# Kernel optimization log

Measured on AMD Instinct MI355X. Metric: run time of the kernel, lower is better.

Reference implementation:

```python
import jax, jax.numpy as jnp
import numpy as np

B = 1
E = 8388608                      # embedding size (dim 1)
NNZ = 131072                     # inhibition links
MIN_SPARSITY = 0.002
MAX_SPARSITY = 0.02
BOOST_PERCENT = 1e-8             # forward default boost_percent
MAX_ACTIVE = int(np.ceil(MAX_SPARSITY * E))    # 167773, torch uses .item() -> static
MIN_ACTIVE = int(np.floor(MIN_SPARSITY * E))   # 16777


def setup_inputs() -> dict:
    key = jax.random.key(0)
    k1, k3, k4, k5 = jax.random.split(key, 4)
    x = jax.random.normal(k1, (B, E, 1, 1), dtype=jnp.float32)
    boost_tensor = jnp.zeros((B, E, 1, 1), dtype=jnp.float32)   # initial boost state (zeros_like in module)
    inh_affector = jax.random.randint(k3, (NNZ,), 0, E, dtype=jnp.int32)
    inh_affectee = jax.random.randint(k4, (NNZ,), 0, E, dtype=jnp.int32)
    # inhibition values are negative (self-inhibition, affect_value=-0.01 scale)
    inh_values = -jax.random.uniform(k5, (NNZ,), dtype=jnp.float32) * 0.05
    return {"x": x, "boost_tensor": boost_tensor, "inh_values": inh_values,
            "inh_affector": inh_affector, "inh_affectee": inh_affectee}


def reference(x, boost_tensor, inh_values, inh_affector, inh_affectee):
    xf = x.reshape(B, E)
    bf = boost_tensor.reshape(B, E)

    # --- run_boosting: PercentClosenessBoosting (units far from max get boosted) ---
    boost_new = bf + (1.0 - xf / jnp.max(xf)) * jnp.float32(BOOST_PERCENT)
    boosted = jnp.maximum(xf, 0.0) + boost_new   # tensor_above + boost_tensor

    # --- apply_sparse_self_affector: tens[affectee] += tens[affector] * values ---
    # RHS gathered from the pre-update tensor, scatter-add onto affectee coords.
    inhibited = boosted.at[0, inh_affectee].add(boosted[0, inh_affector] * inh_values)

    # --- run_k_winners_positive: keep top max_active per row, binarize positives ---
    topv, topi = jax.lax.top_k(inhibited, MAX_ACTIVE)          # [B, K]
    rows = jnp.arange(B)[:, None]
    result = jnp.zeros((B, E), dtype=jnp.float32).at[rows, topi].set(
        (topv > 0).astype(jnp.float32))

    # --- choose_boosted_to_satisfy_minimum ---
    actually_active = jnp.sum(result)
    _, boost_idx = jax.lax.top_k(boost_new, MIN_ACTIVE)        # [B, MIN_ACTIVE]
    to_activate = jnp.ceil(jnp.float32(MIN_ACTIVE) - actually_active)
    need = actually_active < jnp.float32(MIN_ACTIVE)
    add = need & (jnp.arange(MIN_ACTIVE, dtype=jnp.float32) < to_activate)
    add = jnp.broadcast_to(add.astype(jnp.float32), (B, MIN_ACTIVE))
    out = result.at[rows, boost_idx].max(add)

    return out.reshape(B, E, 1, 1)
```

## Files before the change

kernel.cpp:

```cpp
#include <hip/hip_runtime.h>
#include <stdint.h>

#define E_SIZE   8388608
#define N4       (E_SIZE / 4)
#define NNZ_SZ   131072
#define K_ACT    167773
#define MIN_ACT  16777
#define CAP      262144
#define BCAP     2048
#define TINY_F   9.5367431640625e-7f
#define NBINS    16384
#define SHIFT1   18
#define SEL_LDS  32768


__device__ __forceinline__ unsigned int f2A(float f) {
    unsigned int u = __float_as_uint(f);
    return (u & 0x80000000u) ? ~u : (u | 0x80000000u);
}
__device__ __forceinline__ unsigned int f2D(float f) { return ~f2A(f); }
__device__ __forceinline__ float A2f(unsigned int A) {
    unsigned int u = (A & 0x80000000u) ? (A & 0x7FFFFFFFu) : ~A;
    return __uint_as_float(u);
}
__device__ __forceinline__ float D2f(unsigned int D) { return A2f(~D); }

__device__ __forceinline__ float boostedf(float v, float b, float mx) {
    return fmaxf(v, 0.0f) + (b + (1.0f - v / mx) * 1e-8f);
}
__device__ __forceinline__ unsigned int binclamp14(float v) {
    return (v < TINY_F) ? (NBINS - 1u) : (f2D(v) >> SHIFT1);
}
__device__ __forceinline__ unsigned int blo_from(float mx) {
    float tlo = 0.25f * mx;
    unsigned int b = (tlo > 0.0f) ? (f2D(tlo) >> SHIFT1) : (NBINS - 1u);
    return min(b, (unsigned int)(NBINS - 1u));
}

__device__ void block_select(const unsigned int* counts, int nbins, unsigned int Krem,
                             unsigned int* res, unsigned int* scratch) {
    int t = threadIdx.x;
    int per = nbins >> 10; if (per == 0) per = 1;
    int nth = nbins / per;
    unsigned int part = 0;
    if (t < nth)
        for (int j = 0; j < per; j++) part += counts[t * per + j];
    scratch[t] = part;
    unsigned int ws = part;
    for (int off = 32; off; off >>= 1) ws += __shfl_down(ws, off, 64);
    if ((t & 63) == 0) scratch[1024 + (t >> 6)] = ws;
    __syncthreads();
    if (t == 0) {
        unsigned int cum = 0;
        int w = 0;
        for (; w < 15; w++) {
            unsigned int s = scratch[1024 + w];
            if (cum + s >= Krem) break;
            cum += s;
        }
        int tt = w * 64, te = tt + 63;
        for (; tt < te; tt++) {
            unsigned int s = scratch[tt];
            if (cum + s >= Krem) break;
            cum += s;
        }
        int b = tt * per, be = b + per - 1;
        for (; b < be; b++) {
            unsigned int s = counts[b];
            if (cum + s >= Krem) break;
            cum += s;
        }
        res[0] = (unsigned int)b;
        res[1] = Krem - cum;
    }
    __syncthreads();
}

__global__ void __launch_bounds__(256)
k_max(const float4* __restrict__ x, unsigned int* __restrict__ pmax,
      unsigned int* __restrict__ ctrl, unsigned int* __restrict__ hist) {
    int t = threadIdx.x, blk = blockIdx.x;
    if (blk == 0 && t < 64) ctrl[t] = 0u;
    if (t < 16) hist[blk * 16 + t] = 0u;
    int tid = blk * 256 + t;
    unsigned int m = 0u;
    for (int i = tid; i < N4; i += 1024 * 256) {
        float4 v = x[i];
        m = max(m, f2A(v.x)); m = max(m, f2A(v.y));
        m = max(m, f2A(v.z)); m = max(m, f2A(v.w));
    }
    for (int off = 32; off; off >>= 1)
        m = max(m, __shfl_down(m, off, 64));
    __shared__ unsigned int sm[4];
    if ((t & 63) == 0) sm[t >> 6] = m;
    __syncthreads();
    if (t == 0) pmax[blk] = max(max(sm[0], sm[1]), max(sm[2], sm[3]));
}

__device__ __forceinline__ float reduce_pmax(const unsigned int* __restrict__ pmax,
                                             unsigned int* smax) {
    int t = threadIdx.x;
    unsigned int m = pmax[t];
    for (int off = 32; off; off >>= 1)
        m = max(m, __shfl_down(m, off, 64));
    if ((t & 63) == 0) smax[t >> 6] = m;
    __syncthreads();
    if (t == 0) {
        unsigned int r = smax[0];
        for (int i = 1; i < 16; i++) r = max(r, smax[i]);
        smax[0] = r;
    }
    __syncthreads();
    return A2f(smax[0]);
}

__device__ __forceinline__ float reduce_pmax256(const unsigned int* __restrict__ pmax,
                                                unsigned int* smax) {
    int t = threadIdx.x;
    unsigned int m = max(max(pmax[t], pmax[t + 256]),
                         max(pmax[t + 512], pmax[t + 768]));
    for (int off = 32; off; off >>= 1)
        m = max(m, __shfl_down(m, off, 64));
    if ((t & 63) == 0) smax[t >> 6] = m;
    __syncthreads();
    if (t == 0) smax[0] = max(max(smax[0], smax[1]), max(smax[2], smax[3]));
    __syncthreads();
    return A2f(smax[0]);
}

__global__ void __launch_bounds__(1024)
k_boost_hist(const float4* __restrict__ x, const float4* __restrict__ bf,
             float4* __restrict__ out, const unsigned int* __restrict__ pmax,
             unsigned int* __restrict__ hist) {
    __shared__ unsigned int h[NBINS];
    __shared__ unsigned int smax[16];
    float mx = reduce_pmax(pmax, smax);
    unsigned int b_lo = blo_from(mx);
    int t = threadIdx.x;
    for (unsigned int i = t; i <= b_lo; i += 1024) h[i] = 0u;
    __syncthreads();
    int gtid = blockIdx.x * 1024 + t;
    for (int i = gtid; i < N4; i += 512 * 1024) {
        float4 v = x[i], b = bf[i];
        float4 r;
        r.x = boostedf(v.x, b.x, mx);
        r.y = boostedf(v.y, b.y, mx);
        r.z = boostedf(v.z, b.z, mx);
        r.w = boostedf(v.w, b.w, mx);
        out[i] = r;
        #define HISTONE(c) { unsigned int bc = f2D(c) >> SHIFT1; \
            if (bc <= b_lo) atomicAdd(&h[bc], 1u); }
        HISTONE(r.x); HISTONE(r.y); HISTONE(r.z); HISTONE(r.w);
        #undef HISTONE
    }
    __syncthreads();
    for (unsigned int k = t; k <= b_lo; k += 1024) {
        unsigned int c = h[k];
        if (c) atomicAdd(&hist[k], c);
    }
}

__global__ void __launch_bounds__(256)
k_scatter(const float* __restrict__ x, const float* __restrict__ bf,
          const float* __restrict__ vals, const int* __restrict__ aff,
          const int* __restrict__ afe, float* __restrict__ out,
          const unsigned int* __restrict__ pmax, unsigned int* __restrict__ hist) {
    __shared__ unsigned int smax[16];
    float mx = reduce_pmax256(pmax, smax);
    unsigned int b_lo = blo_from(mx);
    int i = blockIdx.x * 256 + threadIdx.x;
    int a = aff[i], e = afe[i];
    float bo = boostedf(x[a], bf[a], mx);
    float contrib = bo * vals[i];
    float old = atomicAdd(&out[e], contrib);
    float nw = old + contrib;
    unsigned int ob = f2D(old) >> SHIFT1, nb = f2D(nw) >> SHIFT1;
    if (ob != nb) {
        if (nb <= b_lo) atomicAdd(&hist[nb], 1u);
        if (ob <= b_lo) atomicAdd((int*)&hist[ob], -1);
    }
}

__global__ void __launch_bounds__(1024)
k_markscan(float4* __restrict__ out, const unsigned int* __restrict__ hist,
           unsigned int* __restrict__ ctrl, unsigned int* __restrict__ gidx,
           unsigned int* __restrict__ gD) {
    __shared__ unsigned int scratch[1040];
    __shared__ unsigned int res[2];
    __shared__ unsigned int cidx[BCAP];
    __shared__ unsigned int cDs[BCAP];
    __shared__ unsigned int scnt, sbase;
    int t = threadIdx.x;
    block_select(hist, NBINS, (unsigned int)K_ACT, res, scratch);
    unsigned int b1 = res[0];
    if (t == 0) {
        scnt = 0;
        if (blockIdx.x == 0) {
            atomicExch(&ctrl[32], res[0]);
            atomicExch(&ctrl[33], res[1]);
        }
    }
    __syncthreads();
    int gtid = blockIdx.x * 1024 + t;
    for (int i = gtid; i < N4; i += 512 * 1024) {
        float4 f = out[i];
        float4 r;
        #define MARKONE(c, rr, comp) { \
            unsigned int bc = binclamp14(c); \
            if (bc < b1) rr = ((c) > 0.0f) ? 1.0f : 0.0f; \
            else { rr = 0.0f; if (bc == b1) { \
                unsigned int p = atomicAdd(&scnt, 1u); \
                if (p < BCAP) { cidx[p] = (unsigned int)i * 4u + comp; cDs[p] = f2D(c); } } } }
        MARKONE(f.x, r.x, 0u); MARKONE(f.y, r.y, 1u);
        MARKONE(f.z, r.z, 2u); MARKONE(f.w, r.w, 3u);
        #undef MARKONE
        out[i] = r;
    }
    __syncthreads();
    if (t == 0) {
        unsigned int m = min(scnt, (unsigned int)BCAP);
        scnt = m;
        sbase = atomicAdd(&ctrl[7], m);
    }
    __syncthreads();
    unsigned int m = scnt, base = sbase;
    for (unsigned int i = t; i < m; i += 1024) {
        unsigned int g = base + i;
        if (g < CAP) { gidx[g] = cidx[i]; gD[g] = cDs[i]; }
    }
}

__global__ void __launch_bounds__(1024)
k_select(float* __restrict__ out, const unsigned int* __restrict__ ctrl,
         const unsigned int* __restrict__ gidx, const unsigned int* __restrict__ gD) {
    __shared__ unsigned int sD[SEL_LDS];
    __shared__ unsigned int h512[512];
    __shared__ unsigned int scratch[1040];
    __shared__ unsigned int res[2];
    __shared__ unsigned int ties[128];
    __shared__ unsigned int tcnt;
    int t = threadIdx.x;
    unsigned int nc = min(ctrl[7], (unsigned int)CAP);
    unsigned int b1 = ctrl[32];
    unsigned int Krem = ctrl[33];
    unsigned int ns = min(nc, (unsigned int)SEL_LDS);

    for (unsigned int i = t; i < ns; i += 1024) sD[i] = gD[i];
    if (t < 512) h512[t] = 0u;
    if (t == 0) tcnt = 0u;
    __syncthreads();
    #define GETD(i) (((i) < ns) ? sD[(i)] : gD[(i)])

    for (unsigned int i = t; i < nc; i += 1024)
        atomicAdd(&h512[(GETD(i) >> 9) & 511u], 1u);
    __syncthreads();
    block_select(h512, 512, Krem, res, scratch);
    unsigned int b2 = res[0], Krem2 = res[1];

    if (t < 512) h512[t] = 0u;
    __syncthreads();
    for (unsigned int i = t; i < nc; i += 1024) {
        unsigned int D = GETD(i);
        if (((D >> 9) & 511u) == b2) atomicAdd(&h512[D & 511u], 1u);
    }
    __syncthreads();
    block_select(h512, 512, Krem2, res, scratch);
    unsigned int b3 = res[0], need = res[1];
    unsigned int T = (b1 << SHIFT1) | (b2 << 9) | b3;

    for (unsigned int i = t; i < nc; i += 1024) {
        if (GETD(i) == T) {
            unsigned int p = atomicAdd(&tcnt, 1u);
            if (p < 128) ties[p] = gidx[i];
        }
    }
    __syncthreads();
    unsigned int M = min(tcnt, 128u);
    float val = (D2f(T) > 0.0f) ? 1.0f : 0.0f;
    for (unsigned int i = t; i < M; i += 1024) {
        unsigned int idx = ties[i];
        unsigned int rank = 0;
        for (unsigned int j = 0; j < M; j++) rank += (ties[j] < idx) ? 1u : 0u;
        if (rank < need) out[idx] = val;
    }
    for (unsigned int i = t; i < nc; i += 1024) {
        unsigned int D = GETD(i);
        if (D < T) out[gidx[i]] = (D2f(D) > 0.0f) ? 1.0f : 0.0f;
    }
    #undef GETD
}

extern "C" void kernel_launch(void* const* d_in, const int* in_sizes, int n_in,
                              void* d_out, int out_size, void* d_ws, size_t ws_size,
                              hipStream_t stream) {
    const float* x    = (const float*)d_in[0];
    const float* bf   = (const float*)d_in[1];
    const float* vals = (const float*)d_in[2];
    const int*   aff  = (const int*)d_in[3];
    const int*   afe  = (const int*)d_in[4];
    float* out = (float*)d_out;

    unsigned int* ctrl = (unsigned int*)d_ws;
    unsigned int* pmax = (unsigned int*)((char*)d_ws + 4096);
    unsigned int* hist = (unsigned int*)((char*)d_ws + 8192);
    unsigned int* gidx = (unsigned int*)((char*)d_ws + 8192 + (size_t)NBINS * 4);
    unsigned int* gD   = (unsigned int*)((char*)d_ws + 8192 + (size_t)NBINS * 4 + (size_t)CAP * 4);

    k_max<<<1024, 256, 0, stream>>>((const float4*)x, pmax, ctrl, hist);
    k_boost_hist<<<512, 1024, 0, stream>>>((const float4*)x, (const float4*)bf,
                                           (float4*)out, pmax, hist);
    k_scatter<<<512, 256, 0, stream>>>(x, bf, vals, aff, afe, out, pmax, hist);
    k_markscan<<<512, 1024, 0, stream>>>((float4*)out, hist, ctrl, gidx, gD);
    k_select<<<1, 1024, 0, stream>>>(out, ctrl, gidx, gD);
}
```

Baseline: 196.3 us.

## Drop histogram fixup from scatter; widen candidate band and count marked exactly

The scatter kernel no longer keeps the coarse histogram in sync with its value-returning atomic adds. Instead it does a plain fire-and-forget atomic add. To tolerate the now-approximate histogram, markscan collects candidates from bins b1 and b1+1, counts the positives it actually marks into a global counter, and the select kernel derives the remaining count from that exact tally over a 1024-bin relative histogram. This removes returning atomics and extra histogram atomics from scatter. The risk is that a stale histogram could shift elements across more than one bin and overflow the candidate capacity.

```diff
diff --git a/kernel.cpp b/kernel.cpp
--- a/kernel.cpp
+++ b/kernel.cpp
@@ -164,21 +164,13 @@
 k_scatter(const float* __restrict__ x, const float* __restrict__ bf,
           const float* __restrict__ vals, const int* __restrict__ aff,
           const int* __restrict__ afe, float* __restrict__ out,
-          const unsigned int* __restrict__ pmax, unsigned int* __restrict__ hist) {
+          const unsigned int* __restrict__ pmax) {
     __shared__ unsigned int smax[16];
     float mx = reduce_pmax256(pmax, smax);
-    unsigned int b_lo = blo_from(mx);
     int i = blockIdx.x * 256 + threadIdx.x;
     int a = aff[i], e = afe[i];
     float bo = boostedf(x[a], bf[a], mx);
-    float contrib = bo * vals[i];
-    float old = atomicAdd(&out[e], contrib);
-    float nw = old + contrib;
-    unsigned int ob = f2D(old) >> SHIFT1, nb = f2D(nw) >> SHIFT1;
-    if (ob != nb) {
-        if (nb <= b_lo) atomicAdd(&hist[nb], 1u);
-        if (ob <= b_lo) atomicAdd((int*)&hist[ob], -1);
-    }
+    atomicAdd(&out[e], bo * vals[i]);
 }
 
 __global__ void __launch_bounds__(1024)
@@ -189,26 +181,26 @@
     __shared__ unsigned int res[2];
     __shared__ unsigned int cidx[BCAP];
     __shared__ unsigned int cDs[BCAP];
+    __shared__ unsigned int smk[16];
     __shared__ unsigned int scnt, sbase;
     int t = threadIdx.x;
     block_select(hist, NBINS, (unsigned int)K_ACT, res, scratch);
     unsigned int b1 = res[0];
+    unsigned int b1p1 = min(b1 + 1u, (unsigned int)(NBINS - 1));
     if (t == 0) {
         scnt = 0;
-        if (blockIdx.x == 0) {
-            atomicExch(&ctrl[32], res[0]);
-            atomicExch(&ctrl[33], res[1]);
-        }
-    }
-    __syncthreads();
+        if (blockIdx.x == 0) atomicExch(&ctrl[32], b1);
+    }
+    __syncthreads();
+    unsigned int mk = 0;
     int gtid = blockIdx.x * 1024 + t;
     for (int i = gtid; i < N4; i += 512 * 1024) {
         float4 f = out[i];
         float4 r;
         #define MARKONE(c, rr, comp) { \
             unsigned int bc = binclamp14(c); \
-            if (bc < b1) rr = ((c) > 0.0f) ? 1.0f : 0.0f; \
-            else { rr = 0.0f; if (bc == b1) { \
+            if (bc < b1) { rr = ((c) > 0.0f) ? 1.0f : 0.0f; mk += ((c) > 0.0f) ? 1u : 0u; } \
+            else { rr = 0.0f; if (bc <= b1p1) { \
                 unsigned int p = atomicAdd(&scnt, 1u); \
                 if (p < BCAP) { cidx[p] = (unsigned int)i * 4u + comp; cDs[p] = f2D(c); } } } }
         MARKONE(f.x, r.x, 0u); MARKONE(f.y, r.y, 1u);
@@ -216,8 +208,13 @@
         #undef MARKONE
         out[i] = r;
     }
+    for (int off = 32; off; off >>= 1) mk += __shfl_down(mk, off, 64);
+    if ((t & 63) == 0) smk[t >> 6] = mk;
     __syncthreads();
     if (t == 0) {
+        unsigned int s = 0;
+        for (int i = 0; i < 16; i++) s += smk[i];
+        atomicAdd(&ctrl[40], s);
         unsigned int m = min(scnt, (unsigned int)BCAP);
         scnt = m;
         sbase = atomicAdd(&ctrl[7], m);
@@ -234,7 +231,7 @@
 k_select(float* __restrict__ out, const unsigned int* __restrict__ ctrl,
          const unsigned int* __restrict__ gidx, const unsigned int* __restrict__ gD) {
     __shared__ unsigned int sD[SEL_LDS];
-    __shared__ unsigned int h512[512];
+    __shared__ unsigned int h[1024];
     __shared__ unsigned int scratch[1040];
     __shared__ unsigned int res[2];
     __shared__ unsigned int ties[128];
@@ -242,31 +239,33 @@
     int t = threadIdx.x;
     unsigned int nc = min(ctrl[7], (unsigned int)CAP);
     unsigned int b1 = ctrl[32];
-    unsigned int Krem = ctrl[33];
+    unsigned int marked = ctrl[40];
+    unsigned int Krem = (unsigned int)K_ACT - marked;
+    unsigned int kb = b1 << SHIFT1;
     unsigned int ns = min(nc, (unsigned int)SEL_LDS);
 
     for (unsigned int i = t; i < ns; i += 1024) sD[i] = gD[i];
-    if (t < 512) h512[t] = 0u;
+    h[t] = 0u;
     if (t == 0) tcnt = 0u;
     __syncthreads();
     #define GETD(i) (((i) < ns) ? sD[(i)] : gD[(i)])
 
     for (unsigned int i = t; i < nc; i += 1024)
-        atomicAdd(&h512[(GETD(i) >> 9) & 511u], 1u);
-    __syncthreads();
-    block_select(h512, 512, Krem, res, scratch);
+        atomicAdd(&h[(GETD(i) - kb) >> 9], 1u);
+    __syncthreads();
+    block_select(h, 1024, Krem, res, scratch);
     unsigned int b2 = res[0], Krem2 = res[1];
 
-    if (t < 512) h512[t] = 0u;
+    if (t < 512) h[t] = 0u;
     __syncthreads();
     for (unsigned int i = t; i < nc; i += 1024) {
-        unsigned int D = GETD(i);
-        if (((D >> 9) & 511u) == b2) atomicAdd(&h512[D & 511u], 1u);
-    }
-    __syncthreads();
-    block_select(h512, 512, Krem2, res, scratch);
+        unsigned int key = GETD(i) - kb;
+        if ((key >> 9) == b2) atomicAdd(&h[key & 511u], 1u);
+    }
+    __syncthreads();
+    block_select(h, 512, Krem2, res, scratch);
     unsigned int b3 = res[0], need = res[1];
-    unsigned int T = (b1 << SHIFT1) | (b2 << 9) | b3;
+    unsigned int T = kb + (b2 << 9) + b3;
 
     for (unsigned int i = t; i < nc; i += 1024) {
         if (GETD(i) == T) {
@@ -309,7 +308,7 @@
     k_max<<<1024, 256, 0, stream>>>((const float4*)x, pmax, ctrl, hist);
     k_boost_hist<<<512, 1024, 0, stream>>>((const float4*)x, (const float4*)bf,
                                            (float4*)out, pmax, hist);
-    k_scatter<<<512, 256, 0, stream>>>(x, bf, vals, aff, afe, out, pmax, hist);
+    k_scatter<<<512, 256, 0, stream>>>(x, bf, vals, aff, afe, out, pmax);
     k_markscan<<<512, 1024, 0, stream>>>((float4*)out, hist, ctrl, gidx, gD);
     k_select<<<1, 1024, 0, stream>>>(out, ctrl, gidx, gD);
 }
```

After: 189.7 us. 3.3% less time.
